# Kernel tuning notes

Measured on AMD Instinct MI355X. Metric: run time of the kernel, lower is better.

## Reference

```python
import jax, jax.numpy as jnp
import numpy as np

N = 20000          # nodes
E = 640000         # edges
IN_F, CL1_F, CL2_F, OUT_F = 128, 256, 128, 10
K = 4              # Chebyshev order
EPS = 1e-5         # BatchNorm eps
LAMBDA_MAX = 2.0   # PyG ChebConv default


def setup_inputs() -> dict:
    key = jax.random.key(0)
    ks = jax.random.split(key, 8)
    x = jax.random.normal(ks[0], (N, IN_F), dtype=jnp.float32)
    edge_index = jax.random.randint(ks[1], (2, E), 0, N, dtype=jnp.int64)
    edge_weight = jax.random.uniform(ks[2], (E,), dtype=jnp.float32)
    W1 = jax.random.normal(ks[3], (K, IN_F, CL1_F), dtype=jnp.float32) * 0.05
    b1 = jnp.zeros((CL1_F,), jnp.float32)
    W2 = jax.random.normal(ks[4], (K, CL1_F, CL2_F), dtype=jnp.float32) * 0.05
    b2 = jnp.zeros((CL2_F,), jnp.float32)
    gamma1 = jnp.ones((CL1_F,), jnp.float32); beta1 = jnp.zeros((CL1_F,), jnp.float32)
    gamma2 = jnp.ones((CL2_F,), jnp.float32); beta2 = jnp.zeros((CL2_F,), jnp.float32)
    Wlin = jax.random.normal(ks[5], (OUT_F, CL2_F), dtype=jnp.float32) * 0.05
    blin = jnp.zeros((OUT_F,), jnp.float32)
    return {"x": x, "edge_index": edge_index, "edge_weight": edge_weight,
            "W1": W1, "b1": b1, "W2": W2, "b2": b2,
            "gamma1": gamma1, "beta1": beta1, "gamma2": gamma2, "beta2": beta2,
            "Wlin": Wlin, "blin": blin}


def _cheb_norm(edge_index, edge_weight, n):
    # Scaled Laplacian L_hat = (2/lambda_max) * (I - D^{-1/2} A D^{-1/2}) - I
    # (matches PyG ChebConv __norm__ with normalization='sym').
    row, col = edge_index[0], edge_index[1]
    w = jnp.where(row == col, 0.0, edge_weight)  # remove_self_loops
    deg = jax.ops.segment_sum(w, row, num_segments=n)
    dis = jnp.where(deg > 0, 1.0 / jnp.sqrt(deg), 0.0)
    w_norm = -(dis[row] * w * dis[col]) * (2.0 / LAMBDA_MAX)
    diag_w = 2.0 / LAMBDA_MAX - 1.0  # = 0 for lambda_max=2
    return row, col, w_norm, diag_w


def _cheb_conv(x, row, col, w_norm, diag_w, W, b):
    n = x.shape[0]

    def spmm(t):  # L_hat @ t : gather sources, scale, scatter-add to targets
        return jax.ops.segment_sum(w_norm[:, None] * t[row], col, num_segments=n) + diag_w * t

    Tx0 = x
    out = Tx0 @ W[0]
    Tx1 = spmm(Tx0)
    out = out + Tx1 @ W[1]
    for k in range(2, W.shape[0]):  # Chebyshev recursion T_k = 2 L_hat T_{k-1} - T_{k-2}
        Tx2 = 2.0 * spmm(Tx1) - Tx0
        out = out + Tx2 @ W[k]
        Tx0, Tx1 = Tx1, Tx2
    return out + b


def _batchnorm(x, gamma, beta):  # training-mode BN over the node axis
    m = x.mean(axis=0)
    v = x.var(axis=0)
    return gamma * (x - m) / jnp.sqrt(v + EPS) + beta


def reference(x, edge_index, edge_weight, W1, b1, W2, b2,
              gamma1, beta1, gamma2, beta2, Wlin, blin):
    row, col, w_norm, diag_w = _cheb_norm(edge_index, edge_weight, x.shape[0])
    h = jax.nn.relu(_cheb_conv(x, row, col, w_norm, diag_w, W1, b1))
    h = _batchnorm(h, gamma1, beta1)
    h = jax.nn.relu(_cheb_conv(h, row, col, w_norm, diag_w, W2, b2))
    h = _batchnorm(h, gamma2, beta2)
    return h @ Wlin.T + blin  # [N, OUT_F]
```

## Files before the change

kernel.cpp:

```cpp
#include <hip/hip_runtime.h>
#include <cstdint>
#include <cstddef>

#define NNODES 20000
#define NEDGES 640000
#define IN_F   128
#define CL1_F  256
#define CL2_F  128
#define OUT_F  10
#define BN_EPS 1e-5f

#define NC     256
#define CE     (NEDGES / NC)
#define HALFN  10000

#define CONVN  (512 * 256 + 4 * 256 * 128 + NNODES * 128)

typedef unsigned short u16;


__device__ __forceinline__ float bf2f(u16 u) {
    union { uint32_t i; float f; } v; v.i = ((uint32_t)u) << 16; return v.f;
}
__device__ __forceinline__ u16 f2bf(float f) {
    union { float f; uint32_t i; } v; v.f = f;
    uint32_t r = v.i + 0x7fffu + ((v.i >> 16) & 1u);
    return (u16)(r >> 16);
}
__device__ __forceinline__ void bf2x2(uint32_t u, float& lo, float& hi) {
    union { uint32_t i; float f; } a, b;
    a.i = u << 16; b.i = u & 0xffff0000u;
    lo = a.f; hi = b.f;
}
__device__ __forceinline__ uint32_t f2bf2(float lo, float hi) {
    return (uint32_t)f2bf(lo) | ((uint32_t)f2bf(hi) << 16);
}
__device__ __forceinline__ void unpack8(uint4 v, float* o) {
    bf2x2(v.x, o[0], o[1]); bf2x2(v.y, o[2], o[3]);
    bf2x2(v.z, o[4], o[5]); bf2x2(v.w, o[6], o[7]);
}


__launch_bounds__(256)
__global__ void build_hist_conv(const int* __restrict__ ei, const float* __restrict__ ew,
                                u16* __restrict__ cnt_h, u16* __restrict__ degq_h,
                                const float* __restrict__ W1, u16* __restrict__ W1t,
                                const float* __restrict__ W2, u16* __restrict__ W2t,
                                const float* __restrict__ x, u16* __restrict__ A1,
                                int E, int N) {
    __shared__ uint32_t scnt[HALFN / 2];
    __shared__ uint32_t sdeg[HALFN / 2];
    int b = blockIdx.x;
    if (b < NC) {
        int e0 = b * CE, e1 = e0 + CE;
        for (int half = 0; half < 2; ++half) {
            int lo = half * HALFN;
            for (int i = threadIdx.x; i < HALFN / 2; i += 256) { scnt[i] = 0; sdeg[i] = 0; }
            __syncthreads();
            for (int e = e0 + threadIdx.x; e < e1; e += 256) {
                int r = ei[e];
                int c = ei[E + e];
                int ci = c - lo;
                if ((unsigned)ci < HALFN) atomicAdd(&scnt[ci >> 1], 1u << ((ci & 1) * 16));
                int ri = r - lo;
                if ((unsigned)ri < HALFN) {
                    float w = (r == c) ? 0.0f : ew[e];
                    uint32_t q = (uint32_t)(w * 1024.0f + 0.5f);
                    atomicAdd(&sdeg[ri >> 1], q << ((ri & 1) * 16));
                }
            }
            __syncthreads();
            for (int i = threadIdx.x; i < HALFN; i += 256) {
                cnt_h[(size_t)b * N + lo + i]  = (u16)((scnt[i >> 1] >> ((i & 1) * 16)) & 0xffffu);
                degq_h[(size_t)b * N + lo + i] = (u16)((sdeg[i >> 1] >> ((i & 1) * 16)) & 0xffffu);
            }
            __syncthreads();
        }
    } else {
        int i = (b - NC) * 256 + threadIdx.x;
        const int S1 = 512 * 256;
        const int S2 = 4 * 256 * 128;
        const int SX = NNODES * 128;
        if (i < S1) {
            int k = i / 256, n = i - k * 256;
            W1t[(size_t)n * 512 + k] = f2bf(W1[i]);
        } else if (i < S1 + S2) {
            int j = i - S1;
            int kc = j / (256 * 128);
            int rem = j - kc * 256 * 128;
            int ci = rem / 128, co = rem - ci * 128;
            W2t[(size_t)(kc * 128 + co) * 256 + ci] = f2bf(W2[j]);
        } else if (i < S1 + S2 + SX) {
            int j = i - S1 - S2;
            int n = j >> 7, f = j & 127;
            A1[(size_t)n * 512 + f] = f2bf(x[j]);
        }
    }
}

__global__ void reduce_dis_base(const u16* __restrict__ cnt_h, const u16* __restrict__ degq_h,
                                int* __restrict__ tot, float* __restrict__ dis,
                                u16* __restrict__ baseD, int N) {
    int i = blockIdx.x * blockDim.x + threadIdx.x;
    if (i >= N) return;
    int t = 0;
    uint32_t dq = 0;
#pragma unroll 8
    for (int c = 0; c < NC; ++c) {
        baseD[(size_t)c * N + i] = (u16)t;
        t  += cnt_h[(size_t)c * N + i];
        dq += degq_h[(size_t)c * N + i];
    }
    tot[i] = t;
    float d = (float)dq * (1.0f / 1024.0f);
    dis[i] = (d > 0.0f) ? rsqrtf(d) : 0.0f;
}

__global__ void scan_kernel(const int* __restrict__ tot, int* __restrict__ rowptr, int N) {
    __shared__ int sums[256];
    int t = threadIdx.x;
    int per = (N + 255) / 256;
    int s0 = t * per, s1 = min(s0 + per, N);
    int s = 0;
    for (int i = s0; i < s1; ++i) s += tot[i];
    sums[t] = s;
    __syncthreads();
    if (t == 0) {
        int run = 0;
        for (int i = 0; i < 256; ++i) { int v = sums[i]; sums[i] = run; run += v; }
        rowptr[N] = run;
    }
    __syncthreads();
    int run = sums[t];
    for (int i = s0; i < s1; ++i) { rowptr[i] = run; run += tot[i]; }
}

__launch_bounds__(256)
__global__ void fill_kernel(const int* __restrict__ ei, const float* __restrict__ ew,
                            const float* __restrict__ dis, const int* __restrict__ rowptr,
                            const u16* __restrict__ baseD,
                            uint32_t* __restrict__ erec, int E, int N) {
    __shared__ uint32_t srank[NNODES / 2];
    int chunk = blockIdx.x;
    int e0 = chunk * CE, e1 = e0 + CE;
    for (int i = threadIdx.x; i < NNODES / 2; i += 256) srank[i] = 0;
    __syncthreads();
    for (int e = e0 + threadIdx.x; e < e1; e += 256) {
        int r = ei[e];
        int c = ei[E + e];
        float w = (r == c) ? 0.0f : ew[e];
        float wn = -(dis[r] * w * dis[c]);
        int sh = (c & 1) * 16;
        uint32_t old = atomicAdd(&srank[c >> 1], 1u << sh);
        int rank = (old >> sh) & 0xffff;
        int pos = rowptr[c] + (int)baseD[(size_t)chunk * N + c] + rank;
        erec[pos] = (uint32_t)r | ((uint32_t)f2bf(wn) << 16);
    }
}

__launch_bounds__(256)
__global__ void spmm_cl(const int* __restrict__ rowptr, const uint32_t* __restrict__ erec,
                        const u16* __restrict__ tin, int ldi,
                        const u16* __restrict__ t1, int ld1, float c1,
                        const u16* __restrict__ t2, int ld2, float c2,
                        u16* __restrict__ tout, int ldo,
                        const float* __restrict__ bias, int doReluBias,
                        int N, float s) {
    int gid = blockIdx.x * blockDim.x + threadIdx.x;
    int n = gid >> 4;
    if (n >= N) return;
    int f = (gid & 15) << 3;
    int p = rowptr[n], pe = rowptr[n + 1];
    float acc[8] = {};
    for (; p + 7 < pe; p += 8) {
        uint32_t rr[8];
#pragma unroll
        for (int u = 0; u < 8; ++u) rr[u] = erec[p + u];
        uint4 vv[8];
#pragma unroll
        for (int u = 0; u < 8; ++u)
            vv[u] = *(const uint4*)(tin + (size_t)(rr[u] & 0xffffu) * ldi + f);
#pragma unroll
        for (int u = 0; u < 8; ++u) {
            float w = bf2f((u16)(rr[u] >> 16));
            float fa[8];
            unpack8(vv[u], fa);
#pragma unroll
            for (int q = 0; q < 8; ++q) acc[q] += w * fa[q];
        }
    }
    for (; p < pe; ++p) {
        uint32_t r0 = erec[p];
        uint4 v0 = *(const uint4*)(tin + (size_t)(r0 & 0xffffu) * ldi + f);
        float w0 = bf2f((u16)(r0 >> 16));
        float fa[8];
        unpack8(v0, fa);
#pragma unroll
        for (int q = 0; q < 8; ++q) acc[q] += w0 * fa[q];
    }
#pragma unroll
    for (int q = 0; q < 8; ++q) acc[q] *= s;
    if (t1) {
        uint4 v = *(const uint4*)(t1 + (size_t)n * ld1 + f);
        float fv[8]; unpack8(v, fv);
#pragma unroll
        for (int q = 0; q < 8; ++q) acc[q] += c1 * fv[q];
    }
    if (t2) {
        uint4 v = *(const uint4*)(t2 + (size_t)n * ld2 + f);
        float fv[8]; unpack8(v, fv);
#pragma unroll
        for (int q = 0; q < 8; ++q) acc[q] += c2 * fv[q];
    }
    if (doReluBias) {
#pragma unroll
        for (int q = 0; q < 8; ++q) acc[q] = fmaxf(acc[q] + bias[f + q], 0.0f);
    }
    uint4 o;
    o.x = f2bf2(acc[0], acc[1]);
    o.y = f2bf2(acc[2], acc[3]);
    o.z = f2bf2(acc[4], acc[5]);
    o.w = f2bf2(acc[6], acc[7]);
    *(uint4*)(tout + (size_t)n * ldo + f) = o;
}


typedef __attribute__((ext_vector_type(8))) short short8;
typedef __attribute__((ext_vector_type(4))) float floatx4;

#define GBM 64
#define GBN 64
#define GBK 64

__launch_bounds__(256)
__global__ void gemm_mfma(const u16* __restrict__ A, const u16* __restrict__ Bt,
                          const float* __restrict__ bias, void* __restrict__ Cout,
                          float* __restrict__ ssum, float* __restrict__ ssq,
                          int M, int N, int K, int doRelu, int outBf) {
    __shared__ __align__(16) u16 As[GBM][GBK + 8];
    __shared__ __align__(16) u16 Bs[GBN][GBK + 8];
    __shared__ float colsum[GBN], colsq[GBN];

    int tid = threadIdx.x;
    int lane = tid & 63;
    int wave = tid >> 6;
    int wm = (wave & 1) * 32;
    int wn = (wave >> 1) * 32;
    int rowBase = blockIdx.x * GBM;
    int colBase = blockIdx.y * GBN;

    floatx4 acc[2][2];
#pragma unroll
    for (int i = 0; i < 2; ++i)
#pragma unroll
        for (int j = 0; j < 2; ++j) {
            acc[i][j][0] = 0.f; acc[i][j][1] = 0.f; acc[i][j][2] = 0.f; acc[i][j][3] = 0.f;
        }

    int sr = tid >> 3;
    int sc = (tid & 7) * 8;

    for (int k0 = 0; k0 < K; k0 += GBK) {
#pragma unroll
        for (int h = 0; h < 2; ++h) {
            int r = sr + h * 32;
            int gm = rowBase + r;
            uint4 v = make_uint4(0, 0, 0, 0);
            if (gm < M) v = *(const uint4*)(A + (size_t)gm * K + k0 + sc);
            *(uint4*)&As[r][sc] = v;
            int gn = colBase + r;
            uint4 w = *(const uint4*)(Bt + (size_t)gn * K + k0 + sc);
            *(uint4*)&Bs[r][sc] = w;
        }
        __syncthreads();

        int mrow = lane & 15;
        int kq = (lane >> 4) * 8;
#pragma unroll
        for (int kk = 0; kk < GBK; kk += 32) {
            short8 af[2], bfr[2];
#pragma unroll
            for (int i = 0; i < 2; ++i) af[i] = *(const short8*)&As[wm + i * 16 + mrow][kk + kq];
#pragma unroll
            for (int j = 0; j < 2; ++j) bfr[j] = *(const short8*)&Bs[wn + j * 16 + mrow][kk + kq];
#pragma unroll
            for (int i = 0; i < 2; ++i)
#pragma unroll
                for (int j = 0; j < 2; ++j)
                    acc[i][j] = __builtin_amdgcn_mfma_f32_16x16x32_bf16(af[i], bfr[j], acc[i][j], 0, 0, 0);
        }
        __syncthreads();
    }

    if (ssum) {
        if (tid < GBN) { colsum[tid] = 0.f; colsq[tid] = 0.f; }
        __syncthreads();
    }

    int cn0 = colBase + wn + (lane & 15);
    int rq = (lane >> 4) * 4;
    float* Cf = (float*)Cout;
    u16*   Cb = (u16*)Cout;
#pragma unroll
    for (int j = 0; j < 2; ++j) {
        float ps = 0.f, pq = 0.f;
        int n = cn0 + j * 16;
#pragma unroll
        for (int i = 0; i < 2; ++i) {
#pragma unroll
            for (int r = 0; r < 4; ++r) {
                int m = rowBase + wm + i * 16 + rq + r;
                if (m >= M) continue;
                float v = acc[i][j][r];
                if (bias) v += bias[n];
                if (doRelu) v = fmaxf(v, 0.0f);
                if (outBf) {
                    u16 bb = f2bf(v);
                    Cb[(size_t)m * N + n] = bb;
                    if (ssum) { float vb = bf2f(bb); ps += vb; pq += vb * vb; }
                } else {
                    Cf[(size_t)m * N + n] = v;
                }
            }
        }
        if (ssum) {
            int lc = wn + j * 16 + (lane & 15);
            atomicAdd(&colsum[lc], ps);
            atomicAdd(&colsq[lc], pq);
        }
    }
    if (ssum) {
        __syncthreads();
        if (tid < GBN) {
            atomicAdd(&ssum[colBase + tid], colsum[tid]);
            atomicAdd(&ssq[colBase + tid], colsq[tid]);
        }
    }
}


#define BN_ROWS 64
__global__ void bn_stats_bf(const u16* __restrict__ h, int N, int C,
                            float* __restrict__ sums, float* __restrict__ sumsq) {
    int c = threadIdx.x;
    int r0 = blockIdx.x * BN_ROWS;
    int r1 = min(r0 + BN_ROWS, N);
    float s = 0.f, q = 0.f;
    for (int r = r0; r < r1; ++r) {
        float v = bf2f(h[(size_t)r * C + c]);
        s += v;
        q += v * v;
    }
    atomicAdd(&sums[c], s);
    atomicAdd(&sumsq[c], q);
}

__launch_bounds__(256)
__global__ void fold_w2(u16* __restrict__ W2t, const float* __restrict__ sums,
                        const float* __restrict__ sumsq, const float* __restrict__ gamma,
                        const float* __restrict__ beta, float* __restrict__ rowvec, float invN) {
    __shared__ float red[4];
    int n = blockIdx.x;
    int k = threadIdx.x;
    float m = sums[k] * invN;
    float var = sumsq[k] * invN - m * m;
    float sc = gamma[k] / sqrtf(var + BN_EPS);
    float sh = beta[k] - m * sc;
    float wf = bf2f(W2t[(size_t)n * 256 + k]);
    W2t[(size_t)n * 256 + k] = f2bf(wf * sc);
    float part = sh * wf;
#pragma unroll
    for (int off = 32; off > 0; off >>= 1) part += __shfl_down(part, off);
    if ((k & 63) == 0) red[k >> 6] = part;
    __syncthreads();
    if (k == 0) rowvec[n] = red[0] + red[1] + red[2] + red[3];
}


__global__ void final_linear_bn(const u16* __restrict__ g, const float* __restrict__ Wlin,
                                const float* __restrict__ blin, const float* __restrict__ sums,
                                const float* __restrict__ sumsq, const float* __restrict__ gamma,
                                const float* __restrict__ beta, float* __restrict__ out,
                                int N, float invN) {
    __shared__ float Ws[OUT_F * CL2_F];
    __shared__ float bs[OUT_F];
    __shared__ float scs[CL2_F], shs[CL2_F];
    for (int i = threadIdx.x; i < OUT_F * CL2_F; i += 256) Ws[i] = Wlin[i];
    if (threadIdx.x < OUT_F) bs[threadIdx.x] = blin[threadIdx.x];
    if (threadIdx.x < CL2_F) {
        int c = threadIdx.x;
        float m = sums[c] * invN;
        float var = sumsq[c] * invN - m * m;
        float sc = gamma[c] / sqrtf(var + BN_EPS);
        scs[c] = sc;
        shs[c] = beta[c] - m * sc;
    }
    __syncthreads();
    int idx = blockIdx.x * 256 + threadIdx.x;
    if (idx >= N * OUT_F) return;
    int n = idx / OUT_F, o = idx - n * OUT_F;
    const u16* gr = g + (size_t)n * CL2_F;
    const float* wr = Ws + o * CL2_F;
    float acc = 0.f;
#pragma unroll 8
    for (int f = 0; f < CL2_F; ++f) acc += (bf2f(gr[f]) * scs[f] + shs[f]) * wr[f];
    out[idx] = acc + bs[o];
}


extern "C" void kernel_launch(void* const* d_in, const int* in_sizes, int n_in,
                              void* d_out, int out_size, void* d_ws, size_t ws_size,
                              hipStream_t stream) {
    const float* x      = (const float*)d_in[0];
    const int*   ei     = (const int*)d_in[1];
    const float* ew     = (const float*)d_in[2];
    const float* W1     = (const float*)d_in[3];
    const float* b1     = (const float*)d_in[4];
    const float* W2     = (const float*)d_in[5];
    const float* b2     = (const float*)d_in[6];
    const float* gamma1 = (const float*)d_in[7];
    const float* beta1  = (const float*)d_in[8];
    const float* gamma2 = (const float*)d_in[9];
    const float* beta2  = (const float*)d_in[10];
    const float* Wlin   = (const float*)d_in[11];
    const float* blin   = (const float*)d_in[12];
    float* out = (float*)d_out;

    const int N = NNODES, E = NEDGES;

    char* base = (char*)d_ws;
    u16*     cnt_h  = (u16*)    (base + 0);
    u16*     degq_h = (u16*)    (base + 10240000);
    u16*     baseD  = (u16*)    (base + 20480000);
    u16*     A1     = (u16*)    (base + 30720000);
    u16*     Hc     = A1;
    u16*     h1bf   = (u16*)    (base + 51200000);
    u16*     pbuf   = (u16*)    (base + 61440000);
    u16*     bb2    = (u16*)    (base + 66560000);
    u16*     bb1    = (u16*)    (base + 71680000);
    uint32_t* erec  = (uint32_t*)(base + 76800000);
    u16*     W1t    = (u16*)    (base + 79360000);
    u16*     W2t    = (u16*)    (base + 79622144);
    float*   rowvec = (float*)  (base + 79884288);
    int*     rowptr = (int*)    (base + 79886336);
    int*     tot    = (int*)    (base + 79966352);
    float*   dis    = (float*)  (base + 80046352);
    float*   bns1   = (float*)  (base + 80126352);
    float*   bnq1    = bns1 + 256;
    float*   bns2    = bnq1 + 256;
    float*   bnq2    = bns2 + 256;

    dim3 blk(256);

    hipMemsetAsync(bns1, 0, 4 * 256 * sizeof(float), stream);

    build_hist_conv<<<dim3(NC + (CONVN + 255) / 256), blk, 0, stream>>>(
        ei, ew, cnt_h, degq_h, W1, W1t, W2, W2t, x, A1, E, N);
    reduce_dis_base<<<dim3((N + 255) / 256), blk, 0, stream>>>(cnt_h, degq_h, tot, dis, baseD, N);
    scan_kernel<<<dim3(1), blk, 0, stream>>>(tot, rowptr, N);
    fill_kernel<<<dim3(NC), blk, 0, stream>>>(ei, ew, dis, rowptr, baseD, erec, E, N);

    dim3 gS(((N << 4) + 255) / 256);

    spmm_cl<<<gS, blk, 0, stream>>>(rowptr, erec, A1 + 0,   512, nullptr,  512, 0.f,
                                    nullptr, 512, 0.f, A1 + 128, 512, nullptr, 0, N, 1.0f);
    spmm_cl<<<gS, blk, 0, stream>>>(rowptr, erec, A1 + 128, 512, A1 + 0,   512, -1.f,
                                    nullptr, 512, 0.f, A1 + 256, 512, nullptr, 0, N, 2.0f);
    spmm_cl<<<gS, blk, 0, stream>>>(rowptr, erec, A1 + 256, 512, A1 + 128, 512, -1.f,
                                    nullptr, 512, 0.f, A1 + 384, 512, nullptr, 0, N, 2.0f);

    gemm_mfma<<<dim3((N + GBM - 1) / GBM, CL1_F / GBN), blk, 0, stream>>>(
        A1, W1t, b1, h1bf, bns1, bnq1, N, CL1_F, 512, 1, 1);

    fold_w2<<<dim3(512), dim3(256), 0, stream>>>(W2t, bns1, bnq1, gamma1, beta1, rowvec, 1.0f / N);

    gemm_mfma<<<dim3((N + GBM - 1) / GBM, 512 / GBN), blk, 0, stream>>>(
        h1bf, W2t, rowvec, Hc, nullptr, nullptr, N, 512, 256, 0, 1);

    spmm_cl<<<gS, blk, 0, stream>>>(rowptr, erec, Hc + 384, 512, Hc + 256, 512, 1.f,
                                    nullptr, 512, 0.f, bb2, 128, nullptr, 0, N, 2.0f);
    spmm_cl<<<gS, blk, 0, stream>>>(rowptr, erec, bb2, 128, Hc + 384, 512, -1.f,
                                    Hc + 128, 512, 1.f, bb1, 128, nullptr, 0, N, 2.0f);
    spmm_cl<<<gS, blk, 0, stream>>>(rowptr, erec, bb1, 128, bb2, 128, -1.f,
                                    Hc + 0, 512, 1.f, pbuf, 128, b2, 1, N, 1.0f);

    bn_stats_bf<<<dim3((N + BN_ROWS - 1) / BN_ROWS), dim3(CL2_F), 0, stream>>>(pbuf, N, CL2_F, bns2, bnq2);

    final_linear_bn<<<dim3((N * OUT_F + 255) / 256), blk, 0, stream>>>(
        pbuf, Wlin, blin, bns2, bnq2, gamma2, beta2, out, N, 1.0f / N);
}
```

Before: 379.7 us.

## Build CSR with global atomics instead of per-chunk shared histograms

Replaces the chunked shared-memory histogram, per-chunk base reduction and rank-based fill with direct global atomic counting of in-degree and weighted out-degree, followed by an atomic-cursor fill. This removes the large per-chunk count and degree arrays and the reduction kernel that read them, cutting memory traffic and one launch. The x-to-bf16 conversion is vectorised, and the final linear folds the batchnorm scale and shift into the weights with vector loads. Edge order within each column becomes nondeterministic, so float summation order can vary between runs.

```diff
diff --git a/kernel.cpp b/kernel.cpp
--- a/kernel.cpp
+++ b/kernel.cpp
@@ -10,11 +10,9 @@
 #define OUT_F  10
 #define BN_EPS 1e-5f
 
-#define NC     256
-#define CE     (NEDGES / NC)
-#define HALFN  10000
-
-#define CONVN  (512 * 256 + 4 * 256 * 128 + NNODES * 128)
+#define EB (NEDGES / 256)
+#define WB 512
+#define XB ((NNODES * 16) / 256)
 
 typedef unsigned short u16;
 
@@ -42,81 +40,43 @@
 
 
 __launch_bounds__(256)
-__global__ void build_hist_conv(const int* __restrict__ ei, const float* __restrict__ ew,
-                                u16* __restrict__ cnt_h, u16* __restrict__ degq_h,
-                                const float* __restrict__ W1, u16* __restrict__ W1t,
-                                const float* __restrict__ W2, u16* __restrict__ W2t,
-                                const float* __restrict__ x, u16* __restrict__ A1,
-                                int E, int N) {
-    __shared__ uint32_t scnt[HALFN / 2];
-    __shared__ uint32_t sdeg[HALFN / 2];
-    int b = blockIdx.x;
-    if (b < NC) {
-        int e0 = b * CE, e1 = e0 + CE;
-        for (int half = 0; half < 2; ++half) {
-            int lo = half * HALFN;
-            for (int i = threadIdx.x; i < HALFN / 2; i += 256) { scnt[i] = 0; sdeg[i] = 0; }
-            __syncthreads();
-            for (int e = e0 + threadIdx.x; e < e1; e += 256) {
-                int r = ei[e];
-                int c = ei[E + e];
-                int ci = c - lo;
-                if ((unsigned)ci < HALFN) atomicAdd(&scnt[ci >> 1], 1u << ((ci & 1) * 16));
-                int ri = r - lo;
-                if ((unsigned)ri < HALFN) {
-                    float w = (r == c) ? 0.0f : ew[e];
-                    uint32_t q = (uint32_t)(w * 1024.0f + 0.5f);
-                    atomicAdd(&sdeg[ri >> 1], q << ((ri & 1) * 16));
-                }
-            }
-            __syncthreads();
-            for (int i = threadIdx.x; i < HALFN; i += 256) {
-                cnt_h[(size_t)b * N + lo + i]  = (u16)((scnt[i >> 1] >> ((i & 1) * 16)) & 0xffffu);
-                degq_h[(size_t)b * N + lo + i] = (u16)((sdeg[i >> 1] >> ((i & 1) * 16)) & 0xffffu);
-            }
-            __syncthreads();
-        }
+__global__ void count_convert(const int* __restrict__ ei, const float* __restrict__ ew,
+                              int* __restrict__ tot, float* __restrict__ degf,
+                              const float* __restrict__ W1, u16* __restrict__ W1t,
+                              const float* __restrict__ W2, u16* __restrict__ W2t,
+                              const float* __restrict__ x, u16* __restrict__ A1,
+                              int E, int N) {
+    int b = blockIdx.x, tid = threadIdx.x;
+    if (b < EB) {
+        int e = b * 256 + tid;
+        int r = ei[e];
+        int c = ei[E + e];
+        atomicAdd(&tot[c], 1);
+        if (r != c) atomicAdd(&degf[r], ew[e]);
+    } else if (b < EB + WB) {
+        int i = (b - EB) * 256 + tid;
+        int k = i >> 8, n = i & 255;
+        W1t[(size_t)n * 512 + k] = f2bf(W1[i]);
+    } else if (b < EB + 2 * WB) {
+        int j = (b - EB - WB) * 256 + tid;
+        int kc = j / (256 * 128);
+        int rem = j - kc * 256 * 128;
+        int ci = rem >> 7, co = rem & 127;
+        W2t[(size_t)(kc * 128 + co) * 256 + ci] = f2bf(W2[j]);
     } else {
-        int i = (b - NC) * 256 + threadIdx.x;
-        const int S1 = 512 * 256;
-        const int S2 = 4 * 256 * 128;
-        const int SX = NNODES * 128;
-        if (i < S1) {
-            int k = i / 256, n = i - k * 256;
-            W1t[(size_t)n * 512 + k] = f2bf(W1[i]);
-        } else if (i < S1 + S2) {
-            int j = i - S1;
-            int kc = j / (256 * 128);
-            int rem = j - kc * 256 * 128;
-            int ci = rem / 128, co = rem - ci * 128;
-            W2t[(size_t)(kc * 128 + co) * 256 + ci] = f2bf(W2[j]);
-        } else if (i < S1 + S2 + SX) {
-            int j = i - S1 - S2;
-            int n = j >> 7, f = j & 127;
-            A1[(size_t)n * 512 + f] = f2bf(x[j]);
-        }
-    }
-}
-
-__global__ void reduce_dis_base(const u16* __restrict__ cnt_h, const u16* __restrict__ degq_h,
-                                int* __restrict__ tot, float* __restrict__ dis,
-                                u16* __restrict__ baseD, int N) {
-    int i = blockIdx.x * blockDim.x + threadIdx.x;
-    if (i >= N) return;
-    int t = 0;
-    uint32_t dq = 0;
-#pragma unroll 8
-    for (int c = 0; c < NC; ++c) {
-        baseD[(size_t)c * N + i] = (u16)t;
-        t  += cnt_h[(size_t)c * N + i];
-        dq += degq_h[(size_t)c * N + i];
-    }
-    tot[i] = t;
-    float d = (float)dq * (1.0f / 1024.0f);
-    dis[i] = (d > 0.0f) ? rsqrtf(d) : 0.0f;
-}
-
-__global__ void scan_kernel(const int* __restrict__ tot, int* __restrict__ rowptr, int N) {
+        int j = (b - EB - 2 * WB) * 256 + tid;
+        int n = j >> 4, f = (j & 15) << 3;
+        const float4* xp = (const float4*)(x + (size_t)n * 128 + f);
+        float4 v0 = xp[0], v1 = xp[1];
+        uint4 o;
+        o.x = f2bf2(v0.x, v0.y); o.y = f2bf2(v0.z, v0.w);
+        o.z = f2bf2(v1.x, v1.y); o.w = f2bf2(v1.z, v1.w);
+        *(uint4*)(A1 + (size_t)n * 512 + f) = o;
+    }
+}
+
+__global__ void scan_kernel(const int* __restrict__ tot, const float* __restrict__ degf,
+                            int* __restrict__ rowptr, float* __restrict__ dis, int N) {
     __shared__ int sums[256];
     int t = threadIdx.x;
     int per = (N + 255) / 256;
@@ -132,30 +92,24 @@
     }
     __syncthreads();
     int run = sums[t];
-    for (int i = s0; i < s1; ++i) { rowptr[i] = run; run += tot[i]; }
+    for (int i = s0; i < s1; ++i) {
+        rowptr[i] = run; run += tot[i];
+        float d = degf[i];
+        dis[i] = (d > 0.0f) ? rsqrtf(d) : 0.0f;
+    }
 }
 
 __launch_bounds__(256)
 __global__ void fill_kernel(const int* __restrict__ ei, const float* __restrict__ ew,
                             const float* __restrict__ dis, const int* __restrict__ rowptr,
-                            const u16* __restrict__ baseD,
-                            uint32_t* __restrict__ erec, int E, int N) {
-    __shared__ uint32_t srank[NNODES / 2];
-    int chunk = blockIdx.x;
-    int e0 = chunk * CE, e1 = e0 + CE;
-    for (int i = threadIdx.x; i < NNODES / 2; i += 256) srank[i] = 0;
-    __syncthreads();
-    for (int e = e0 + threadIdx.x; e < e1; e += 256) {
-        int r = ei[e];
-        int c = ei[E + e];
-        float w = (r == c) ? 0.0f : ew[e];
-        float wn = -(dis[r] * w * dis[c]);
-        int sh = (c & 1) * 16;
-        uint32_t old = atomicAdd(&srank[c >> 1], 1u << sh);
-        int rank = (old >> sh) & 0xffff;
-        int pos = rowptr[c] + (int)baseD[(size_t)chunk * N + c] + rank;
-        erec[pos] = (uint32_t)r | ((uint32_t)f2bf(wn) << 16);
-    }
+                            int* __restrict__ cursor, uint32_t* __restrict__ erec, int E) {
+    int e = blockIdx.x * 256 + threadIdx.x;
+    int r = ei[e];
+    int c = ei[E + e];
+    float w = (r == c) ? 0.0f : ew[e];
+    float wn = -(dis[r] * w * dis[c]);
+    int pos = rowptr[c] + atomicAdd(&cursor[c], 1);
+    erec[pos] = (uint32_t)r | ((uint32_t)f2bf(wn) << 16);
 }
 
 __launch_bounds__(256)
@@ -377,34 +331,52 @@
 }
 
 
+__launch_bounds__(256)
 __global__ void final_linear_bn(const u16* __restrict__ g, const float* __restrict__ Wlin,
                                 const float* __restrict__ blin, const float* __restrict__ sums,
                                 const float* __restrict__ sumsq, const float* __restrict__ gamma,
                                 const float* __restrict__ beta, float* __restrict__ out,
                                 int N, float invN) {
-    __shared__ float Ws[OUT_F * CL2_F];
-    __shared__ float bs[OUT_F];
+    __shared__ float Ws2[OUT_F][CL2_F + 4];
     __shared__ float scs[CL2_F], shs[CL2_F];
-    for (int i = threadIdx.x; i < OUT_F * CL2_F; i += 256) Ws[i] = Wlin[i];
-    if (threadIdx.x < OUT_F) bs[threadIdx.x] = blin[threadIdx.x];
-    if (threadIdx.x < CL2_F) {
-        int c = threadIdx.x;
-        float m = sums[c] * invN;
-        float var = sumsq[c] * invN - m * m;
-        float sc = gamma[c] / sqrtf(var + BN_EPS);
-        scs[c] = sc;
-        shs[c] = beta[c] - m * sc;
-    }
-    __syncthreads();
-    int idx = blockIdx.x * 256 + threadIdx.x;
+    __shared__ float oc[OUT_F];
+    int tid = threadIdx.x;
+    if (tid < CL2_F) {
+        float m = sums[tid] * invN;
+        float var = sumsq[tid] * invN - m * m;
+        float sc = gamma[tid] / sqrtf(var + BN_EPS);
+        scs[tid] = sc;
+        shs[tid] = beta[tid] - m * sc;
+    }
+    __syncthreads();
+    for (int i = tid; i < OUT_F * CL2_F; i += 256) {
+        int f = i & 127;
+        Ws2[i >> 7][f] = Wlin[i] * scs[f];
+    }
+    __syncthreads();
+    if (tid < OUT_F) {
+        float a = blin[tid];
+        const float* wr = Wlin + tid * CL2_F;
+        for (int f = 0; f < CL2_F; ++f) a += shs[f] * wr[f];
+        oc[tid] = a;
+    }
+    __syncthreads();
+    int idx = blockIdx.x * 256 + tid;
     if (idx >= N * OUT_F) return;
     int n = idx / OUT_F, o = idx - n * OUT_F;
     const u16* gr = g + (size_t)n * CL2_F;
-    const float* wr = Ws + o * CL2_F;
+    const float* w2 = Ws2[o];
     float acc = 0.f;
-#pragma unroll 8
-    for (int f = 0; f < CL2_F; ++f) acc += (bf2f(gr[f]) * scs[f] + shs[f]) * wr[f];
-    out[idx] = acc + bs[o];
+#pragma unroll
+    for (int f0 = 0; f0 < CL2_F; f0 += 8) {
+        uint4 v = *(const uint4*)(gr + f0);
+        float fa[8]; unpack8(v, fa);
+        const float4* wp = (const float4*)(w2 + f0);
+        float4 wa = wp[0], wb = wp[1];
+        acc += fa[0] * wa.x + fa[1] * wa.y + fa[2] * wa.z + fa[3] * wa.w
+             + fa[4] * wb.x + fa[5] * wb.y + fa[6] * wb.z + fa[7] * wb.w;
+    }
+    out[idx] = acc + oc[o];
 }
 
 
@@ -429,36 +401,34 @@
     const int N = NNODES, E = NEDGES;
 
     char* base = (char*)d_ws;
-    u16*     cnt_h  = (u16*)    (base + 0);
-    u16*     degq_h = (u16*)    (base + 10240000);
-    u16*     baseD  = (u16*)    (base + 20480000);
-    u16*     A1     = (u16*)    (base + 30720000);
+    u16*     A1     = (u16*)    (base + 0);
     u16*     Hc     = A1;
-    u16*     h1bf   = (u16*)    (base + 51200000);
-    u16*     pbuf   = (u16*)    (base + 61440000);
-    u16*     bb2    = (u16*)    (base + 66560000);
-    u16*     bb1    = (u16*)    (base + 71680000);
-    uint32_t* erec  = (uint32_t*)(base + 76800000);
-    u16*     W1t    = (u16*)    (base + 79360000);
-    u16*     W2t    = (u16*)    (base + 79622144);
-    float*   rowvec = (float*)  (base + 79884288);
-    int*     rowptr = (int*)    (base + 79886336);
-    int*     tot    = (int*)    (base + 79966352);
-    float*   dis    = (float*)  (base + 80046352);
-    float*   bns1   = (float*)  (base + 80126352);
-    float*   bnq1    = bns1 + 256;
-    float*   bns2    = bnq1 + 256;
-    float*   bnq2    = bns2 + 256;
+    u16*     h1bf   = (u16*)    (base + 20480000);
+    u16*     pbuf   = (u16*)    (base + 30720000);
+    u16*     bb2    = (u16*)    (base + 35840000);
+    u16*     bb1    = (u16*)    (base + 40960000);
+    uint32_t* erec  = (uint32_t*)(base + 46080000);
+    u16*     W1t    = (u16*)    (base + 48640000);
+    u16*     W2t    = (u16*)    (base + 48902144);
+    float*   rowvec = (float*)  (base + 49164288);
+    int*     rowptr = (int*)    (base + 49166336);
+    int*     tot    = (int*)    (base + 49246340);
+    float*   degf   = (float*)  (base + 49326340);
+    int*     cursor = (int*)    (base + 49406340);
+    float*   bns1   = (float*)  (base + 49486340);
+    float*   bnq1   = bns1 + 256;
+    float*   bns2   = bnq1 + 256;
+    float*   bnq2   = bns2 + 256;
+    float*   dis    = (float*)  (base + 49490436);
 
     dim3 blk(256);
 
-    hipMemsetAsync(bns1, 0, 4 * 256 * sizeof(float), stream);
-
-    build_hist_conv<<<dim3(NC + (CONVN + 255) / 256), blk, 0, stream>>>(
-        ei, ew, cnt_h, degq_h, W1, W1t, W2, W2t, x, A1, E, N);
-    reduce_dis_base<<<dim3((N + 255) / 256), blk, 0, stream>>>(cnt_h, degq_h, tot, dis, baseD, N);
-    scan_kernel<<<dim3(1), blk, 0, stream>>>(tot, rowptr, N);
-    fill_kernel<<<dim3(NC), blk, 0, stream>>>(ei, ew, dis, rowptr, baseD, erec, E, N);
+    hipMemsetAsync(tot, 0, 3 * N * sizeof(int) + 4 * 256 * sizeof(float), stream);
+
+    count_convert<<<dim3(EB + 2 * WB + XB), blk, 0, stream>>>(
+        ei, ew, tot, degf, W1, W1t, W2, W2t, x, A1, E, N);
+    scan_kernel<<<dim3(1), blk, 0, stream>>>(tot, degf, rowptr, dis, N);
+    fill_kernel<<<dim3(EB), blk, 0, stream>>>(ei, ew, dis, rowptr, cursor, erec, E);
 
     dim3 gS(((N << 4) + 255) / 256);
 
```

New measurement: 477.4 us. 1.26x slower.
